# Performance work log

Measured on AMD Instinct MI355X. Metric: run time of the kernel, lower is better.

The kernel has to match this reference:

```python
import jax, jax.numpy as jnp
import numpy as np
from jax.scipy.special import logsumexp

COST_GAMMA = 0.1
MIN_ZERO_GAMMA = 0.1
_CLIP = 1.0 - 1e-7


def setup_inputs() -> dict:
    key = jax.random.key(0)
    k1, k2, k3 = jax.random.split(key, 3)
    B, D, K = 65536, 128, 1024
    xs = jax.random.normal(k1, (B, D), dtype=jnp.float32)
    xs = xs / jnp.linalg.norm(xs, axis=-1, keepdims=True)  # points on sphere S^{D-1}
    mus = jax.random.normal(k2, (D, K), dtype=jnp.float32)  # prototype params (pre-projx)
    alphas = jax.random.uniform(k3, (K,), dtype=jnp.float32)
    return {"xs": xs, "mus": mus, "alphas": alphas}


def reference(xs, mus, alphas):
    # projx: project prototype columns onto the unit sphere
    mus_p = mus / jnp.linalg.norm(mus, axis=0, keepdims=True)  # [D, K]
    # sphere cost: half squared geodesic distance, cdist-like [B, K]
    ip = jnp.clip(xs @ mus_p, -_CLIP, _CLIP)
    costs = 0.5 * jnp.arccos(ip) ** 2 + alphas  # [B, K]
    # softmin over components via stable logsumexp
    F = COST_GAMMA * logsumexp(-costs / COST_GAMMA, axis=1)  # [B]
    # soft min(F, 0): logsumexp over stacked (F, 0) == logaddexp
    F = MIN_ZERO_GAMMA * jnp.logaddexp(-F / MIN_ZERO_GAMMA, 0.0)
    return F
```

## Files before the change

### kernel.cpp

```cpp
#include <hip/hip_runtime.h>
#include <hip/hip_bf16.h>


typedef __attribute__((ext_vector_type(8))) short short8;
typedef __attribute__((ext_vector_type(4))) float f32x4;
typedef __attribute__((ext_vector_type(2))) float f32x2;

#define KP 1024
#define DD 128

__device__ __forceinline__ unsigned int f2bf(float f) {
  unsigned int u = __float_as_uint(f);
  return (u + 0x7FFFu + ((u >> 16) & 1u)) >> 16;
}

__device__ __forceinline__ f32x2 pk_fma(f32x2 a, f32x2 b, f32x2 c) {
  return __builtin_elementwise_fma(a, b, c);
}

__global__ __launch_bounds__(256) void prep_kernel(
    const float* __restrict__ mus, const float* __restrict__ alphas,
    uint4* __restrict__ musbf_sw, float* __restrict__ lw) {
  __shared__ float Vt[128][17];
  __shared__ float psum[4][16];
  __shared__ float inv_s[16];
  const int t = threadIdx.x;
  const int wvp = t >> 6, lnp = t & 63;
  const int c0 = blockIdx.x * 16;

  float vloc[8];
  float s = 0.0f;
  #pragma unroll
  for (int j = 0; j < 8; ++j) {
    const int id = j * 256 + t;
    const int d = id >> 4, c = id & 15;
    float v = mus[d * KP + c0 + c];
    vloc[j] = v;
    Vt[d][c] = v;
    s = fmaf(v, v, s);
  }
  (void)vloc;
  s += __shfl_xor(s, 16, 64);
  s += __shfl_xor(s, 32, 64);
  if (lnp < 16) psum[wvp][lnp] = s;
  __syncthreads();
  if (t < 16) {
    float tot = psum[0][t] + psum[1][t] + psum[2][t] + psum[3][t];
    inv_s[t] = rsqrtf(tot);
    lw[c0 + t] = -14.4269504089f * alphas[c0 + t];
  }
  __syncthreads();

  const int col16 = t & 15, w0 = t >> 4;
  const int col = c0 + col16;
  const float inv = inv_s[col16];
  uint4 o;
  o.x = f2bf(Vt[w0 * 8 + 0][col16] * inv) | (f2bf(Vt[w0 * 8 + 1][col16] * inv) << 16);
  o.y = f2bf(Vt[w0 * 8 + 2][col16] * inv) | (f2bf(Vt[w0 * 8 + 3][col16] * inv) << 16);
  o.z = f2bf(Vt[w0 * 8 + 4][col16] * inv) | (f2bf(Vt[w0 * 8 + 5][col16] * inv) << 16);
  o.w = f2bf(Vt[w0 * 8 + 6][col16] * inv) | (f2bf(Vt[w0 * 8 + 7][col16] * inv) << 16);
  musbf_sw[((col >> 6) << 10) + (w0 << 6) + (col & 63)] = o;
}

__global__ __launch_bounds__(256, 4) void main_kernel(
    const float* __restrict__ xs, const uint4* __restrict__ musbf_sw,
    const float* __restrict__ lw, float* __restrict__ out) {
  __shared__ __align__(16) unsigned short Bs[2][8192];
  const int t = threadIdx.x;
  const int wv = t >> 6, ln = t & 63, q = ln >> 4, l15 = ln & 15;

  const int row = blockIdx.x * 64 + wv * 16 + l15;
  const float4* xs4 = (const float4*)xs;
  const int base4 = row * 32 + q * 2;
  short8 afr[4];
  #pragma unroll
  for (int kkk = 0; kkk < 4; ++kkk) {
    float4 f0 = xs4[base4 + kkk * 8];
    float4 f1 = xs4[base4 + kkk * 8 + 1];
    union { short8 s; uint4 u; } a;
    a.u.x = f2bf(f0.x) | (f2bf(f0.y) << 16);
    a.u.y = f2bf(f0.z) | (f2bf(f0.w) << 16);
    a.u.z = f2bf(f1.x) | (f2bf(f1.y) << 16);
    a.u.w = f2bf(f1.z) | (f2bf(f1.w) << 16);
    afr[kkk] = a.s;
  }

  uint4 v[4];
  #pragma unroll
  for (int i = 0; i < 4; ++i) v[i] = musbf_sw[i * 256 + t];
  #pragma unroll
  for (int i = 0; i < 4; ++i) *(uint4*)&Bs[0][(i * 256 + t) * 8] = v[i];
  __syncthreads();

  const f32x2 C_mh = {-0.5f, -0.5f}, C_ph = {0.5f, 0.5f};
  const f32x2 C_z0 = {0.0f, 0.0f};
  const f32x2 C5 = {-3.6067376f, -3.6067376f};
  const f32x2 C4 = {-2.3449500f, -2.3449500f};
  const f32x2 C3 = {-3.2975886f, -3.2975886f};
  const f32x2 C2 = {-5.1295823f, -5.1295823f};
  const f32x2 C1 = {-9.6179669f, -9.6179669f};
  const f32x2 C0 = {-28.8539008f, -28.8539008f};

  f32x2 sums2[2] = {(f32x2){0.f, 0.f}, (f32x2){0.f, 0.f}};

  for (int cg = 0; cg < 16; ++cg) {
    if (cg < 15) {
      #pragma unroll
      for (int i = 0; i < 4; ++i)
        v[i] = musbf_sw[(cg + 1) * 1024 + i * 256 + t];
    }
    float lwv[4];
    #pragma unroll
    for (int nt = 0; nt < 4; ++nt) lwv[nt] = lw[cg * 64 + nt * 16 + l15];

    f32x4 acc[4];
    #pragma unroll
    for (int nt = 0; nt < 4; ++nt) acc[nt] = (f32x4){0.f, 0.f, 0.f, 0.f};
    const unsigned short* bp = &Bs[cg & 1][q * 512 + l15 * 8];
    #pragma unroll
    for (int kkk = 0; kkk < 4; ++kkk)
      #pragma unroll
      for (int nt = 0; nt < 4; ++nt) {
        short8 b = *(const short8*)(bp + kkk * 2048 + nt * 128);
        acc[nt] = __builtin_amdgcn_mfma_f32_16x16x32_bf16(afr[kkk], b, acc[nt], 0, 0, 0);
      }

    #pragma unroll
    for (int nt = 0; nt < 4; ++nt) {
      f32x2 lwp = {lwv[nt], lwv[nt]};
      #pragma unroll
      for (int p = 0; p < 2; ++p) {
        f32x2 x = {acc[nt][2 * p], acc[nt][2 * p + 1]};
        f32x2 z = pk_fma(x, C_mh, C_ph);
        z = __builtin_elementwise_max(z, C_z0);
        f32x2 h = pk_fma(z, C5, C4);
        h = pk_fma(z, h, C3);
        h = pk_fma(z, h, C2);
        h = pk_fma(z, h, C1);
        h = pk_fma(z, h, C0);
        f32x2 arg = pk_fma(z, h, lwp);
        f32x2 e = {__builtin_amdgcn_exp2f(arg.x), __builtin_amdgcn_exp2f(arg.y)};
        sums2[p] = sums2[p] + e;
      }
    }

    if (cg < 15) {
      #pragma unroll
      for (int i = 0; i < 4; ++i)
        *(uint4*)&Bs[(cg + 1) & 1][(i * 256 + t) * 8] = v[i];
      __syncthreads();
    }
  }

  float s[4] = {sums2[0].x, sums2[0].y, sums2[1].x, sums2[1].y};
  #pragma unroll
  for (int s2 = 1; s2 < 16; s2 <<= 1)
    #pragma unroll
    for (int r = 0; r < 4; ++r) s[r] += __shfl_xor(s[r], s2, 64);
  if (l15 == 0) {
    #pragma unroll
    for (int r = 0; r < 4; ++r)
      out[blockIdx.x * 64 + wv * 16 + q * 4 + r] = 0.1f * log1pf(1.0f / s[r]);
  }
}

extern "C" void kernel_launch(void* const* d_in, const int* in_sizes, int n_in,
                              void* d_out, int out_size, void* d_ws, size_t ws_size,
                              hipStream_t stream) {
  const float* xs     = (const float*)d_in[0];
  const float* mus    = (const float*)d_in[1];
  const float* alphas = (const float*)d_in[2];
  float* out = (float*)d_out;

  uint4* musbf_sw = (uint4*)d_ws;
  float* lw = (float*)((char*)d_ws + 16384 * sizeof(uint4));

  prep_kernel<<<KP / 16, 256, 0, stream>>>(mus, alphas, musbf_sw, lw);
  const int B = in_sizes[0] / DD;
  main_kernel<<<B / 64, 256, 0, stream>>>(xs, musbf_sw, lw, out);
}
```

Baseline: 109.5 us.

## Split prototype dimension across two blocks with atomic reduction and finalize kernel

Each row block now handles only half of the 1024 prototypes. The grid doubles, and each block uses half the shared memory and fewer accumulators, with launch bounds raised to target 8 blocks per CU. Partial exp sums are combined with atomicAdd into a zeroed output, and a separate finalize kernel applies the log1p transform. This is meant to raise occupancy and parallelism, at the cost of reloading and converting xs twice, an extra memset and kernel launch, and atomic traffic.

After: 109.8 us. Within noise of the previous version (+0.3%).

```diff
diff --git a/kernel.cpp b/kernel.cpp
--- a/kernel.cpp
+++ b/kernel.cpp
@@ -28,18 +28,15 @@
   const int wvp = t >> 6, lnp = t & 63;
   const int c0 = blockIdx.x * 16;
 
-  float vloc[8];
   float s = 0.0f;
   #pragma unroll
   for (int j = 0; j < 8; ++j) {
     const int id = j * 256 + t;
     const int d = id >> 4, c = id & 15;
     float v = mus[d * KP + c0 + c];
-    vloc[j] = v;
     Vt[d][c] = v;
     s = fmaf(v, v, s);
   }
-  (void)vloc;
   s += __shfl_xor(s, 16, 64);
   s += __shfl_xor(s, 32, 64);
   if (lnp < 16) psum[wvp][lnp] = s;
@@ -62,14 +59,16 @@
   musbf_sw[((col >> 6) << 10) + (w0 << 6) + (col & 63)] = o;
 }
 
-__global__ __launch_bounds__(256, 4) void main_kernel(
+__global__ __launch_bounds__(256, 8) void main_kernel(
     const float* __restrict__ xs, const uint4* __restrict__ musbf_sw,
     const float* __restrict__ lw, float* __restrict__ out) {
-  __shared__ __align__(16) unsigned short Bs[2][8192];
+  __shared__ __align__(16) unsigned short Bs[2][4096];
   const int t = threadIdx.x;
   const int wv = t >> 6, ln = t & 63, q = ln >> 4, l15 = ln & 15;
+  const int rblk = blockIdx.x >> 1;
+  const int ch = blockIdx.x & 1;
 
-  const int row = blockIdx.x * 64 + wv * 16 + l15;
+  const int row = rblk * 64 + wv * 16 + l15;
   const float4* xs4 = (const float4*)xs;
   const int base4 = row * 32 + q * 2;
   short8 afr[4];
@@ -85,11 +84,15 @@
     afr[kkk] = a.s;
   }
 
-  uint4 v[4];
+  const int ci0 = ch * 16;
+  uint4 v[2];
   #pragma unroll
-  for (int i = 0; i < 4; ++i) v[i] = musbf_sw[i * 256 + t];
+  for (int i = 0; i < 2; ++i) {
+    const int u = i * 256 + t;
+    v[i] = musbf_sw[((ci0 >> 1) << 10) + ((u >> 5) << 6) + ((ci0 & 1) << 5) + (u & 31)];
+  }
   #pragma unroll
-  for (int i = 0; i < 4; ++i) *(uint4*)&Bs[0][(i * 256 + t) * 8] = v[i];
+  for (int i = 0; i < 2; ++i) *(uint4*)&Bs[0][(i * 256 + t) * 8] = v[i];
   __syncthreads();
 
   const f32x2 C_mh = {-0.5f, -0.5f}, C_ph = {0.5f, 0.5f};
@@ -103,30 +106,34 @@
 
   f32x2 sums2[2] = {(f32x2){0.f, 0.f}, (f32x2){0.f, 0.f}};
 
-  for (int cg = 0; cg < 16; ++cg) {
-    if (cg < 15) {
+  for (int cgi = 0; cgi < 16; ++cgi) {
+    const int ci = ci0 + cgi;
+    if (cgi < 15) {
+      const int cn = ci + 1;
       #pragma unroll
-      for (int i = 0; i < 4; ++i)
-        v[i] = musbf_sw[(cg + 1) * 1024 + i * 256 + t];
+      for (int i = 0; i < 2; ++i) {
+        const int u = i * 256 + t;
+        v[i] = musbf_sw[((cn >> 1) << 10) + ((u >> 5) << 6) + ((cn & 1) << 5) + (u & 31)];
+      }
     }
-    float lwv[4];
+    float lwv[2];
     #pragma unroll
-    for (int nt = 0; nt < 4; ++nt) lwv[nt] = lw[cg * 64 + nt * 16 + l15];
+    for (int nt = 0; nt < 2; ++nt) lwv[nt] = lw[ci * 32 + nt * 16 + l15];
 
-    f32x4 acc[4];
+    f32x4 acc[2];
     #pragma unroll
-    for (int nt = 0; nt < 4; ++nt) acc[nt] = (f32x4){0.f, 0.f, 0.f, 0.f};
-    const unsigned short* bp = &Bs[cg & 1][q * 512 + l15 * 8];
+    for (int nt = 0; nt < 2; ++nt) acc[nt] = (f32x4){0.f, 0.f, 0.f, 0.f};
+    const unsigned short* bp = &Bs[cgi & 1][q * 256 + l15 * 8];
     #pragma unroll
     for (int kkk = 0; kkk < 4; ++kkk)
       #pragma unroll
-      for (int nt = 0; nt < 4; ++nt) {
-        short8 b = *(const short8*)(bp + kkk * 2048 + nt * 128);
+      for (int nt = 0; nt < 2; ++nt) {
+        short8 b = *(const short8*)(bp + kkk * 1024 + nt * 128);
         acc[nt] = __builtin_amdgcn_mfma_f32_16x16x32_bf16(afr[kkk], b, acc[nt], 0, 0, 0);
       }
 
     #pragma unroll
-    for (int nt = 0; nt < 4; ++nt) {
+    for (int nt = 0; nt < 2; ++nt) {
       f32x2 lwp = {lwv[nt], lwv[nt]};
       #pragma unroll
       for (int p = 0; p < 2; ++p) {
@@ -144,10 +151,10 @@
       }
     }
 
-    if (cg < 15) {
+    if (cgi < 15) {
       #pragma unroll
-      for (int i = 0; i < 4; ++i)
-        *(uint4*)&Bs[(cg + 1) & 1][(i * 256 + t) * 8] = v[i];
+      for (int i = 0; i < 2; ++i)
+        *(uint4*)&Bs[(cgi + 1) & 1][(i * 256 + t) * 8] = v[i];
       __syncthreads();
     }
   }
@@ -160,8 +167,14 @@
   if (l15 == 0) {
     #pragma unroll
     for (int r = 0; r < 4; ++r)
-      out[blockIdx.x * 64 + wv * 16 + q * 4 + r] = 0.1f * log1pf(1.0f / s[r]);
+      atomicAdd(&out[rblk * 64 + wv * 16 + q * 4 + r], s[r]);
   }
+}
+
+__global__ __launch_bounds__(256) void fin_kernel(float* __restrict__ out) {
+  const int i = blockIdx.x * 256 + threadIdx.x;
+  float S = out[i];
+  out[i] = 0.1f * log1pf(1.0f / S);
 }
 
 extern "C" void kernel_launch(void* const* d_in, const int* in_sizes, int n_in,
@@ -175,7 +188,10 @@
   uint4* musbf_sw = (uint4*)d_ws;
   float* lw = (float*)((char*)d_ws + 16384 * sizeof(uint4));
 
+  hipMemsetAsync(out, 0, (size_t)out_size * sizeof(float), stream);
+
   prep_kernel<<<KP / 16, 256, 0, stream>>>(mus, alphas, musbf_sw, lw);
   const int B = in_sizes[0] / DD;
-  main_kernel<<<B / 64, 256, 0, stream>>>(xs, musbf_sw, lw, out);
+  main_kernel<<<B / 32, 256, 0, stream>>>(xs, musbf_sw, lw, out);
+  fin_kernel<<<B / 256, 256, 0, stream>>>(out);
 }
```
